# Kernel tuning notes

Measured on AMD Instinct MI355X. Metric: run time of the kernel, lower is better.

Reference implementation:

```python
import jax, jax.numpy as jnp
import numpy as np

N = 50000
E = 625000
D_IN = 128
D_OUT = 128
NEG_SLOPE = 0.01  # torch LeakyReLU default


def setup_inputs() -> dict:
    key = jax.random.key(0)
    k1, k2, k3, k4, k5, k6, k7, k8 = jax.random.split(key, 8)
    features = jax.random.normal(k1, (N, D_IN), dtype=jnp.float32)
    target = jax.random.randint(k2, (E,), 0, N, dtype=jnp.int64)
    neighbor = jax.random.randint(k3, (E,), 0, N, dtype=jnp.int64)
    values = jax.random.uniform(k4, (E,), dtype=jnp.float32)
    # nn.Linear params (kaiming-uniform-ish init: U(-1/sqrt(in), 1/sqrt(in)))
    bound = 1.0 / np.sqrt(D_IN)
    W1 = jax.random.uniform(k5, (D_OUT, D_IN), minval=-bound, maxval=bound, dtype=jnp.float32)
    b1 = jax.random.uniform(k6, (D_OUT,), minval=-bound, maxval=bound, dtype=jnp.float32)
    W2 = jax.random.uniform(k7, (D_OUT, D_IN), minval=-bound, maxval=bound, dtype=jnp.float32)
    b2 = jax.random.uniform(k8, (D_OUT,), minval=-bound, maxval=bound, dtype=jnp.float32)
    return {"features": features, "target": target, "neighbor": neighbor,
            "values": values, "W1": W1, "b1": b1, "W2": W2, "b2": b2}


def reference(features, target, neighbor, values, W1, b1, W2, b2):
    # gather-scale: msg[e] = features[neighbor[e]] * values[e]
    msg = features[neighbor] * values[:, None]              # (E, D_IN)
    # scatter-add into target nodes
    h_neigh = jax.ops.segment_sum(msg, target, num_segments=N)  # (N, D_IN)
    # dual linear fusion + leaky relu
    h = (features + h_neigh) @ W1.T + b1 + (features * h_neigh) @ W2.T + b2
    return jnp.where(h >= 0, h, NEG_SLOPE * h)
```

## Files before the change

### kernel.cpp

```cpp
#include <hip/hip_runtime.h>

#define D 128
#define CAP 32
#define EPT 2
#define NEG_SLOPE 0.01f

typedef float v4f __attribute__((ext_vector_type(4)));
typedef short short8 __attribute__((ext_vector_type(8)));

static __device__ __forceinline__ short f2bf(float f) {
    unsigned u = __float_as_uint(f);
    unsigned r = (u + 0x7fffu + ((u >> 16) & 1u)) >> 16;
    return (short)r;
}
static __device__ __forceinline__ float bflo(unsigned u) { return __uint_as_float(u << 16); }
static __device__ __forceinline__ float bfhi(unsigned u) { return __uint_as_float(u & 0xffff0000u); }
static __device__ __forceinline__ unsigned packbf(float x, float y) {
    return (unsigned)(unsigned short)f2bf(x) | ((unsigned)(unsigned short)f2bf(y) << 16);
}

__global__ __launch_bounds__(256) void convbucket_kernel(const float* __restrict__ feat,
                                                         const float* __restrict__ W1,
                                                         const float* __restrict__ W2,
                                                         const int* __restrict__ tgt,
                                                         const int* __restrict__ nbr,
                                                         const float* __restrict__ vals,
                                                         unsigned* __restrict__ featbf,
                                                         short* __restrict__ Wbf,
                                                         int* __restrict__ deg,
                                                         unsigned* __restrict__ edata,
                                                         int4* __restrict__ ovf,
                                                         int* __restrict__ ovf_cnt,
                                                         int nQuads, int E, int nbB) {
    if ((int)blockIdx.x < nbB) {
        int base = (blockIdx.x * 256 + threadIdx.x) * EPT;
#pragma unroll
        for (int k = 0; k < EPT; k++) {
            int e = base + k;
            if (e < E) {
                int   t = __builtin_nontemporal_load(&tgt[e]);
                int   n = __builtin_nontemporal_load(&nbr[e]);
                float v = __builtin_nontemporal_load(&vals[e]);
                int slot = atomicAdd(&deg[t], 1);
                if (slot < CAP) {
                    unsigned ent = ((unsigned)n << 16) |
                                   (unsigned)(unsigned short)f2bf(v);
                    edata[((unsigned)t << 5) + slot] = ent;
                } else {
                    int o = atomicAdd(ovf_cnt, 1);
                    int4 ov;
                    ov.x = t;
                    ov.y = n;
                    ov.z = __float_as_int(v);
                    ov.w = 0;
                    ovf[o] = ov;
                }
            }
        }
    } else {
        int i = (blockIdx.x - nbB) * 256 + threadIdx.x;
        if (i < nQuads) {
            v4f f = __builtin_nontemporal_load((const v4f*)feat + i);
            uint2 p;
            p.x = packbf(f.x, f.y);
            p.y = packbf(f.z, f.w);
            ((uint2*)featbf)[i] = p;
        }
        if (i < D * D) {
            Wbf[i]         = f2bf(W1[i]);
            Wbf[D * D + i] = f2bf(W2[i]);
        }
    }
}

__global__ __launch_bounds__(256) void gathergemm_kernel(const unsigned* __restrict__ featbf,
                                                         const unsigned* __restrict__ edata,
                                                         const int* __restrict__ deg,
                                                         const int4* __restrict__ ovf,
                                                         const int* __restrict__ ovf_cnt,
                                                         const short* __restrict__ Wbf,
                                                         const float* __restrict__ b1,
                                                         const float* __restrict__ b2,
                                                         float* __restrict__ out,
                                                         int nNodes) {
    __shared__ __align__(16) unsigned sX[2][1024];

    int tid  = threadIdx.x;
    int lane = tid & 63;
    int w    = tid >> 6;
    int m0   = blockIdx.x * 16;
    if (m0 >= nNodes) return;

    int mrow = lane & 15;
    int quad = lane >> 4;

    for (int k = 0; k < 4; k++) {
        int n    = w * 4 + k;
        int node = m0 + n;
        int d    = (node < nNodes) ? deg[node] : 0;
        int dd   = d < CAP ? d : CAP;

        unsigned uf = featbf[(long)min(node, nNodes - 1) * (D / 2) + lane];

        float ax[4] = {0.f, 0.f, 0.f, 0.f};
        float ay[4] = {0.f, 0.f, 0.f, 0.f};

        {
            const unsigned* ep = edata + ((unsigned)node << 5);
            int dm1 = dd - 1;
            for (int j = 0; j < dd; j += 16) {
                unsigned p[16], u[16];
#pragma unroll
                for (int t = 0; t < 16; t++) p[t] = ep[min(j + t, dm1)];
#pragma unroll
                for (int t = 0; t < 16; t++)
                    u[t] = featbf[(long)(p[t] >> 16) * (D / 2) + lane];
                float v[16];
#pragma unroll
                for (int t = 0; t < 16; t++) v[t] = (j + t < dd) ? bflo(p[t]) : 0.0f;
#pragma unroll
                for (int t = 0; t < 16; t++) {
                    ax[t & 3] += bflo(u[t]) * v[t];
                    ay[t & 3] += bfhi(u[t]) * v[t];
                }
            }
        }

        if (d > CAP) {
            int cnt = *ovf_cnt;
            for (int basek = 0; basek < cnt; basek += 64) {
                int kk = basek + lane;
                int t  = (kk < cnt) ? ovf[kk].x : -1;
                unsigned long long m = __ballot(t == node);
                while (m) {
                    int b = __ffsll((long long)m) - 1;
                    m &= m - 1;
                    int4  ov = ovf[basek + b];
                    float v  = __int_as_float(ov.z);
                    unsigned u = featbf[(long)ov.y * (D / 2) + lane];
                    ax[0] += bflo(u) * v;
                    ay[0] += bfhi(u) * v;
                }
            }
        }

        float accx = (ax[0] + ax[1]) + (ax[2] + ax[3]);
        float accy = (ay[0] + ay[1]) + (ay[2] + ay[3]);
        float fx = bflo(uf), fy = bfhi(uf);
        int idx = n * 64 + (((lane >> 2) ^ n) << 2) + (lane & 3);
        sX[0][idx] = packbf(fx + accx, fy + accy);
        sX[1][idx] = packbf(fx * accx, fy * accy);
    }

    __syncthreads();

    int ot0 = w * 2;
    float bias[2];
#pragma unroll
    for (int j = 0; j < 2; j++) {
        int o = (ot0 + j) * 16 + mrow;
        bias[j] = b1[o] + b2[o];
    }

    v4f acc[2];
#pragma unroll
    for (int j = 0; j < 2; j++) acc[j] = (v4f)(0.0f);

#pragma unroll
    for (int s = 0; s < 4; s++) {
        int ck = s * 4 + quad;
        int pp = ck ^ mrow;
        short8 a1 = *(const short8*)(&sX[0][mrow * 64 + pp * 4]);
        short8 a2 = *(const short8*)(&sX[1][mrow * 64 + pp * 4]);
        const short* wp = Wbf + ck * 8;
#pragma unroll
        for (int j = 0; j < 2; j++) {
            int row = (ot0 + j) * 16 + mrow;
            short8 w1 = *(const short8*)(wp + row * D);
            short8 w2 = *(const short8*)(wp + D * D + row * D);
            acc[j] = __builtin_amdgcn_mfma_f32_16x16x32_bf16(a1, w1, acc[j], 0, 0, 0);
            acc[j] = __builtin_amdgcn_mfma_f32_16x16x32_bf16(a2, w2, acc[j], 0, 0, 0);
        }
    }

#pragma unroll
    for (int j = 0; j < 2; j++) {
        int o = (ot0 + j) * 16 + mrow;
#pragma unroll
        for (int r = 0; r < 4; r++) {
            int node = m0 + quad * 4 + r;
            if (node < nNodes) {
                float v = acc[j][r] + bias[j];
                v = (v >= 0.0f) ? v : NEG_SLOPE * v;
                __builtin_nontemporal_store(v, &out[(long)node * D + o]);
            }
        }
    }
}

extern "C" void kernel_launch(void* const* d_in, const int* in_sizes, int n_in,
                              void* d_out, int out_size, void* d_ws, size_t ws_size,
                              hipStream_t stream) {
    const float* feat = (const float*)d_in[0];
    const int*   tgt  = (const int*)d_in[1];
    const int*   nbr  = (const int*)d_in[2];
    const float* vals = (const float*)d_in[3];
    const float* W1   = (const float*)d_in[4];
    const float* b1   = (const float*)d_in[5];
    const float* W2   = (const float*)d_in[6];
    const float* b2   = (const float*)d_in[7];
    float*       out  = (float*)d_out;

    int E      = in_sizes[1];
    int nNodes = out_size / D;

    int*      deg     = (int*)d_ws;
    int*      ovf_cnt = deg + nNodes;
    int4*     ovf     = (int4*)(deg + nNodes + 4);
    unsigned* edata   = (unsigned*)(ovf + E);
    short*    Wbf     = (short*)(edata + (long)nNodes * CAP);
    unsigned* featbf  = (unsigned*)(Wbf + 2 * D * D);

    int nQuads = nNodes * (D / 4);
    int nbB    = (E + 256 * EPT - 1) / (256 * EPT);
    int nbC    = (nQuads + 255) / 256;

    hipMemsetAsync(deg, 0, (size_t)(nNodes + 4) * sizeof(int), stream);
    convbucket_kernel<<<nbB + nbC, 256, 0, stream>>>(feat, W1, W2, tgt, nbr, vals,
                                                     featbf, Wbf, deg, edata, ovf, ovf_cnt,
                                                     nQuads, E, nbB);

    int nTiles = (nNodes + 15) / 16;
    gathergemm_kernel<<<nTiles, 256, 0, stream>>>(featbf, edata, deg, ovf, ovf_cnt,
                                                  Wbf, b1, b2, out, nNodes);
}
```

Baseline: 178.6 us.

## Flatten per-tile edge list and gather with LDS atomics across 8 waves

The gather-GEMM kernel now uses 512 threads per 16-node tile. It builds a prefix-summed flat list of all edges in the tile in shared memory, so each wave handles 8 edges at a time regardless of which node they belong to. Partial sums are accumulated with shared-memory float atomics, which removes the per-node degree imbalance and the padded-lane waste. The cost is many LDS atomics and extra barriers. Each wave now computes a single 16-column MFMA output tile.

```diff
diff --git a/kernel.cpp b/kernel.cpp
--- a/kernel.cpp
+++ b/kernel.cpp
@@ -73,99 +73,123 @@
     }
 }
 
-__global__ __launch_bounds__(256) void gathergemm_kernel(const unsigned* __restrict__ featbf,
-                                                         const unsigned* __restrict__ edata,
-                                                         const int* __restrict__ deg,
-                                                         const int4* __restrict__ ovf,
-                                                         const int* __restrict__ ovf_cnt,
-                                                         const short* __restrict__ Wbf,
-                                                         const float* __restrict__ b1,
-                                                         const float* __restrict__ b2,
-                                                         float* __restrict__ out,
-                                                         int nNodes) {
+__global__ __launch_bounds__(512, 4) void tilegather_kernel(const unsigned* __restrict__ featbf,
+                                                            const unsigned* __restrict__ edata,
+                                                            const int* __restrict__ deg,
+                                                            const int4* __restrict__ ovf,
+                                                            const int* __restrict__ ovf_cnt,
+                                                            const short* __restrict__ Wbf,
+                                                            const float* __restrict__ b1,
+                                                            const float* __restrict__ b2,
+                                                            float* __restrict__ out,
+                                                            int nNodes) {
+    __shared__ float accp[2][16][64];
     __shared__ __align__(16) unsigned sX[2][1024];
+    __shared__ unsigned short entries[16 * CAP];
+    __shared__ int sdeg[16], sdd[16], pfx[17];
 
     int tid  = threadIdx.x;
     int lane = tid & 63;
     int w    = tid >> 6;
     int m0   = blockIdx.x * 16;
-    if (m0 >= nNodes) return;
-
-    int mrow = lane & 15;
-    int quad = lane >> 4;
-
-    for (int k = 0; k < 4; k++) {
-        int n    = w * 4 + k;
-        int node = m0 + n;
-        int d    = (node < nNodes) ? deg[node] : 0;
-        int dd   = d < CAP ? d : CAP;
-
-        unsigned uf = featbf[(long)min(node, nNodes - 1) * (D / 2) + lane];
-
-        float ax[4] = {0.f, 0.f, 0.f, 0.f};
-        float ay[4] = {0.f, 0.f, 0.f, 0.f};
-
-        {
-            const unsigned* ep = edata + ((unsigned)node << 5);
-            int dm1 = dd - 1;
-            for (int j = 0; j < dd; j += 16) {
-                unsigned p[16], u[16];
-#pragma unroll
-                for (int t = 0; t < 16; t++) p[t] = ep[min(j + t, dm1)];
-#pragma unroll
-                for (int t = 0; t < 16; t++)
-                    u[t] = featbf[(long)(p[t] >> 16) * (D / 2) + lane];
-                float v[16];
-#pragma unroll
-                for (int t = 0; t < 16; t++) v[t] = (j + t < dd) ? bflo(p[t]) : 0.0f;
-#pragma unroll
-                for (int t = 0; t < 16; t++) {
-                    ax[t & 3] += bflo(u[t]) * v[t];
-                    ay[t & 3] += bfhi(u[t]) * v[t];
-                }
+
+    {
+        float* z = &accp[0][0][0];
+        for (int i = tid; i < 2048; i += 512) z[i] = 0.0f;
+        if (tid < 16) {
+            int nd = m0 + tid;
+            int d  = (nd < nNodes) ? deg[nd] : 0;
+            sdeg[tid] = d;
+            sdd[tid]  = d < CAP ? d : CAP;
+        }
+    }
+    __syncthreads();
+
+    if (tid == 0) {
+        int s = 0;
+        pfx[0] = 0;
+#pragma unroll
+        for (int i = 0; i < 16; i++) { s += sdd[i]; pfx[i + 1] = s; }
+    }
+    __syncthreads();
+    int tot = pfx[16];
+    if (tid < tot) {
+        int lo = 0, hi = 16;
+        while (hi - lo > 1) {
+            int mid = (lo + hi) >> 1;
+            if (tid >= pfx[mid]) lo = mid; else hi = mid;
+        }
+        entries[tid] = (unsigned short)((lo << 5) | (tid - pfx[lo]));
+    }
+    __syncthreads();
+
+    {
+        unsigned ebase = (unsigned)m0 << 5;
+        int tm1 = tot - 1;
+        for (int k0 = w * 8; k0 < tot; k0 += 64) {
+            int ent[8];
+            unsigned p[8], u[8];
+#pragma unroll
+            for (int t = 0; t < 8; t++) ent[t] = entries[min(k0 + t, tm1)];
+#pragma unroll
+            for (int t = 0; t < 8; t++) p[t] = edata[ebase + (unsigned)ent[t]];
+#pragma unroll
+            for (int t = 0; t < 8; t++)
+                u[t] = featbf[(long)(p[t] >> 16) * (D / 2) + lane];
+#pragma unroll
+            for (int t = 0; t < 8; t++) {
+                float v = (k0 + t < tot) ? bflo(p[t]) : 0.0f;
+                int   n = ent[t] >> 5;
+                atomicAdd(&accp[0][n][lane], bflo(u[t]) * v);
+                atomicAdd(&accp[1][n][lane], bfhi(u[t]) * v);
             }
         }
-
-        if (d > CAP) {
-            int cnt = *ovf_cnt;
+    }
+    __syncthreads();
+
+#pragma unroll
+    for (int q = 0; q < 2; q++) {
+        int n = w * 2 + q;
+        if (sdeg[n] > CAP) {
+            int node = m0 + n;
+            int cnt  = *ovf_cnt;
             for (int basek = 0; basek < cnt; basek += 64) {
                 int kk = basek + lane;
                 int t  = (kk < cnt) ? ovf[kk].x : -1;
-                unsigned long long m = __ballot(t == node);
-                while (m) {
-                    int b = __ffsll((long long)m) - 1;
-                    m &= m - 1;
+                unsigned long long mm = __ballot(t == node);
+                while (mm) {
+                    int b = __ffsll((long long)mm) - 1;
+                    mm &= mm - 1;
                     int4  ov = ovf[basek + b];
                     float v  = __int_as_float(ov.z);
                     unsigned u = featbf[(long)ov.y * (D / 2) + lane];
-                    ax[0] += bflo(u) * v;
-                    ay[0] += bfhi(u) * v;
+                    atomicAdd(&accp[0][n][lane], bflo(u) * v);
+                    atomicAdd(&accp[1][n][lane], bfhi(u) * v);
                 }
             }
         }
-
-        float accx = (ax[0] + ax[1]) + (ax[2] + ax[3]);
-        float accy = (ay[0] + ay[1]) + (ay[2] + ay[3]);
+    }
+    __syncthreads();
+
+#pragma unroll
+    for (int q = 0; q < 2; q++) {
+        int n    = w * 2 + q;
+        int node = m0 + n;
+        unsigned uf = featbf[(long)min(node, nNodes - 1) * (D / 2) + lane];
+        float accx = accp[0][n][lane], accy = accp[1][n][lane];
         float fx = bflo(uf), fy = bfhi(uf);
         int idx = n * 64 + (((lane >> 2) ^ n) << 2) + (lane & 3);
         sX[0][idx] = packbf(fx + accx, fy + accy);
         sX[1][idx] = packbf(fx * accx, fy * accy);
     }
-
-    __syncthreads();
-
-    int ot0 = w * 2;
-    float bias[2];
-#pragma unroll
-    for (int j = 0; j < 2; j++) {
-        int o = (ot0 + j) * 16 + mrow;
-        bias[j] = b1[o] + b2[o];
-    }
-
-    v4f acc[2];
-#pragma unroll
-    for (int j = 0; j < 2; j++) acc[j] = (v4f)(0.0f);
-
+    __syncthreads();
+
+    int mrow = lane & 15;
+    int quad = lane >> 4;
+    int o    = w * 16 + mrow;
+    float bias = b1[o] + b2[o];
+
+    v4f acc = (v4f)(0.0f);
 #pragma unroll
     for (int s = 0; s < 4; s++) {
         int ck = s * 4 + quad;
@@ -173,27 +197,19 @@
         short8 a1 = *(const short8*)(&sX[0][mrow * 64 + pp * 4]);
         short8 a2 = *(const short8*)(&sX[1][mrow * 64 + pp * 4]);
         const short* wp = Wbf + ck * 8;
-#pragma unroll
-        for (int j = 0; j < 2; j++) {
-            int row = (ot0 + j) * 16 + mrow;
-            short8 w1 = *(const short8*)(wp + row * D);
-            short8 w2 = *(const short8*)(wp + D * D + row * D);
-            acc[j] = __builtin_amdgcn_mfma_f32_16x16x32_bf16(a1, w1, acc[j], 0, 0, 0);
-            acc[j] = __builtin_amdgcn_mfma_f32_16x16x32_bf16(a2, w2, acc[j], 0, 0, 0);
-        }
-    }
-
-#pragma unroll
-    for (int j = 0; j < 2; j++) {
-        int o = (ot0 + j) * 16 + mrow;
-#pragma unroll
-        for (int r = 0; r < 4; r++) {
-            int node = m0 + quad * 4 + r;
-            if (node < nNodes) {
-                float v = acc[j][r] + bias[j];
-                v = (v >= 0.0f) ? v : NEG_SLOPE * v;
-                __builtin_nontemporal_store(v, &out[(long)node * D + o]);
-            }
+        short8 w1 = *(const short8*)(wp + o * D);
+        short8 w2 = *(const short8*)(wp + D * D + o * D);
+        acc = __builtin_amdgcn_mfma_f32_16x16x32_bf16(a1, w1, acc, 0, 0, 0);
+        acc = __builtin_amdgcn_mfma_f32_16x16x32_bf16(a2, w2, acc, 0, 0, 0);
+    }
+
+#pragma unroll
+    for (int r = 0; r < 4; r++) {
+        int node = m0 + quad * 4 + r;
+        if (node < nNodes) {
+            float v = acc[r] + bias;
+            v = (v >= 0.0f) ? v : NEG_SLOPE * v;
+            __builtin_nontemporal_store(v, &out[(long)node * D + o]);
         }
     }
 }
@@ -231,6 +247,6 @@
                                                      nQuads, E, nbB);
 
     int nTiles = (nNodes + 15) / 16;
-    gathergemm_kernel<<<nTiles, 256, 0, stream>>>(featbf, edata, deg, ovf, ovf_cnt,
+    tilegather_kernel<<<nTiles, 512, 0, stream>>>(featbf, edata, deg, ovf, ovf_cnt,
                                                   Wbf, b1, b2, out, nNodes);
 }
```

Measured after the change: 579.9 us. 3.25x slower.
